# Optimization experiments

Hardware: AMD Instinct MI355X
Metric: run time of the kernel (lower is better)

The kernel has to match this reference:

```python
import jax, jax.numpy as jnp
import numpy as np

SPIN_LEN = 365
TRAIN_LEN = 200000
ML = 2.9086  # mean of second forcing (hard-coded in the torch module)
SL = 1.898   # std of second forcing (hard-coded in the torch module)


def setup_inputs() -> dict:
    key = jax.random.key(0)
    kx, ky, kp = jax.random.split(key, 3)
    B, S = 262144, 1
    x = jax.random.uniform(kx, (B, S, 2), dtype=jnp.float32)
    y_obs = jax.random.uniform(ky, (B, 1), dtype=jnp.float32)
    ks = jax.random.split(kp, 6)
    return {
        "x": x,
        "y_obs": y_obs,
        "epoch": 1,
        "time_lag": 0,
        "weight_r_yom": jax.random.uniform(ks[0], (1, 1), dtype=jnp.float32),
        "weight_r_yom_gw": jax.random.uniform(ks[1], (1, 1), dtype=jnp.float32),
        "weight_r_ylm": jax.random.uniform(ks[2], (1, 1), dtype=jnp.float32),
        "weight_r_yfm": jax.random.uniform(ks[3], (1, 1), dtype=jnp.float32),
        "bias_b0_ylm": jax.random.uniform(ks[4], (1,), dtype=jnp.float32),
        "weight_b2_ylm": jax.random.uniform(ks[5], (1, 1), dtype=jnp.float32),
    }


def reference(x, y_obs, epoch, time_lag, weight_r_yom, weight_r_yom_gw,
              weight_r_ylm, weight_r_yfm, bias_b0_ylm, weight_b2_ylm):
    # x: [B, S, 2] (batch_first). The torch code transposes to [S, B, 2] and
    # runs b-outer / t-inner loops with state threaded across BOTH loops, so
    # the scan order over flattened steps is b-major, t-minor.
    B, S, _ = x.shape
    dt = x.dtype

    # softmax-like mass-balance gate normalization over the 4 scalar weights
    e_om = jnp.exp(weight_r_yom[0, 0])
    e_gw = jnp.exp(weight_r_yom_gw[0, 0])
    e_lm = jnp.exp(weight_r_ylm[0, 0])
    e_fm = jnp.exp(weight_r_yfm[0, 0])
    denom = e_om + e_gw + e_lm + e_fm
    oo = e_om / denom      # constant output gate
    oogw = e_gw / denom    # constant groundwater gate
    ol1 = e_lm / denom     # loss-gate scale
    b0 = bias_b0_ylm[0]
    wb2 = weight_b2_ylm[0, 0]

    # unbiased std, matching torch.std default
    obsstd = jnp.std(y_obs[SPIN_LEN:TRAIN_LEN], ddof=1)

    xv = x[time_lag:]                       # [B', S, 2] (time_lag is static)
    Bp = B - time_lag
    u1 = xv[..., 0].reshape(-1)             # [B'*S] inflow
    u2 = xv[..., 1].reshape(-1)             # [B'*S] loss forcing

    def step(c, u):
        u1_t, u2_t = u
        ol = ol1 * jax.nn.sigmoid(b0 + (u2_t - ML) / SL * wb2)
        f = 1.0 - oo - ol - oogw
        c_new = f * c + u1_t                # ib = 0 -> full inflow enters
        return c_new, (c, ol, f)

    _, (c_prev, ol_s, f_s) = jax.lax.scan(step, jnp.zeros((), dt), (u1, u2))

    # torch stores outputs every t but overwrites; only last t per b survives,
    # using c_0 (state BEFORE that step) and that step's ol/f.
    c0 = c_prev.reshape(Bp, S)[:, -1]
    olL = ol_s.reshape(Bp, S)[:, -1]
    fL = f_s.reshape(Bp, S)[:, -1]

    def pad(v):  # rows b < time_lag stay zero, shape [B, 1]
        return jnp.pad(v, (time_lag, 0))[:, None]

    h_n = pad(oo * c0)          # bp = 0 so h_n == q_n
    c_n = pad(c0)
    l_n = pad(olL * c0)
    gw_n = pad(oogw * c0)
    bp_n = jnp.zeros((B, 1), dt)
    gate_ib = jnp.zeros((B, 1), dt)
    valid = pad(jnp.ones((Bp,), dt))
    gate_oo = oo * valid
    gate_oogw = oogw * valid
    gate_ol = pad(olL)
    gate_f = pad(fL)
    obs_std = obsstd * valid
    h_nout = jnp.concatenate([h_n, obs_std], axis=1)
    return (h_n, c_n, l_n, gw_n, bp_n, gate_ib, gate_oo, gate_oogw,
            gate_ol, gate_f, h_nout, obs_std)
```

## Files before the change

kernel.cpp:

```cpp
#include <hip/hip_runtime.h>
#include <math.h>

#define SPIN 365
#define TRAINL 200000
#define ML 2.9086f
#define SLINV (1.0f / 1.898f)

#define THREADS 512
#define ITEMS 2
#define CHUNK (THREADS * ITEMS)
#define NW (THREADS / 64)

struct Sc { float oo, oogw, ol1, b0, k; };

__device__ __forceinline__ Sc get_sc(const float* w0, const float* w1,
                                     const float* w2, const float* w3,
                                     const float* b0p, const float* wb2p) {
  float e_om = __expf(w0[0]);
  float e_gw = __expf(w1[0]);
  float e_lm = __expf(w2[0]);
  float e_fm = __expf(w3[0]);
  float denom = e_om + e_gw + e_lm + e_fm;
  Sc s;
  s.oo   = e_om / denom;
  s.oogw = e_gw / denom;
  s.ol1  = e_lm / denom;
  s.b0   = b0p[0];
  s.k    = wb2p[0] * SLINV;
  return s;
}

__device__ __forceinline__ float sigm_fast(float z) {
  return __fdividef(1.0f, 1.0f + __expf(-z));
}


extern "C" __global__ __launch_bounds__(THREADS) void k1(
    const float* __restrict__ x, const float* __restrict__ y,
    const int* __restrict__ tlp,
    const float* __restrict__ w0, const float* __restrict__ w1,
    const float* __restrict__ w2, const float* __restrict__ w3,
    const float* __restrict__ b0p, const float* __restrict__ wb2p,
    float* __restrict__ out, float* __restrict__ ws, int B, int G)
{
  const int g = blockIdx.x, tid = threadIdx.x;
  const int lane = tid & 63, wid = tid >> 6;
  const int tl = tlp[0];
  const Sc sc = get_sc(w0, w1, w2, w3, b0p, wb2p);
  const int base = g * CHUNK + tid * ITEMS;
  const bool full = (base + ITEMS) <= B;

  float u1v[ITEMS], u2v[ITEMS];
  if (full) {
    float4 a = *(const float4*)(x + 2 * (size_t)base);
    u1v[0] = a.x; u2v[0] = a.y; u1v[1] = a.z; u2v[1] = a.w;
  } else {
    for (int j = 0; j < ITEMS; j++) {
      int p = base + j;
      u1v[j] = (p < B) ? x[2*(size_t)p]     : 0.f;
      u2v[j] = (p < B) ? x[2*(size_t)p + 1] : 0.f;
    }
  }

  float P = 1.f, Q = 0.f;
  float olv[ITEMS], fv[ITEMS];
  for (int j = 0; j < ITEMS; j++) {
    int p = base + j;
    float ol = sc.ol1 * sigm_fast(sc.b0 + (u2v[j] - ML) * sc.k);
    float f  = 1.0f - sc.oo - ol - sc.oogw;
    olv[j] = ol; fv[j] = f;
    bool act = (p >= tl) && (p < B);
    if (act) { Q = f * Q + u1v[j]; P *= f; }
  }

  if (full) {
    bool a0 = (base >= tl), a1 = (base + 1 >= tl);
    *(float2*)(out + 4*(size_t)B + base) = make_float2(0.f, 0.f);
    *(float2*)(out + 5*(size_t)B + base) = make_float2(0.f, 0.f);
    *(float2*)(out + 6*(size_t)B + base) = make_float2(a0?sc.oo:0.f,  a1?sc.oo:0.f);
    *(float2*)(out + 7*(size_t)B + base) = make_float2(a0?sc.oogw:0.f,a1?sc.oogw:0.f);
    *(float2*)(out + 8*(size_t)B + base) = make_float2(a0?olv[0]:0.f, a1?olv[1]:0.f);
    *(float2*)(out + 9*(size_t)B + base) = make_float2(a0?fv[0]:0.f,  a1?fv[1]:0.f);
  } else {
    for (int j = 0; j < ITEMS; j++) {
      int p = base + j;
      if (p < B) {
        bool act = (p >= tl);
        out[4*(size_t)B+p] = 0.f;                  out[5*(size_t)B+p] = 0.f;
        out[6*(size_t)B+p] = act ? sc.oo   : 0.f;  out[7*(size_t)B+p] = act ? sc.oogw : 0.f;
        out[8*(size_t)B+p] = act ? olv[j]  : 0.f;  out[9*(size_t)B+p] = act ? fv[j]   : 0.f;
      }
    }
  }

  #pragma unroll
  for (int off = 1; off < 64; off <<= 1) {
    float pL = __shfl_down(P, off);
    float qL = __shfl_down(Q, off);
    Q = pL * Q + qL;
    P = pL * P;
  }

  float s = 0.f, ss = 0.f;
  if (full && base < TRAINL) {
    float2 yv = *(const float2*)(y + base);
    float vv[2] = { yv.x, yv.y };
    for (int j = 0; j < ITEMS; j++) {
      int p = base + j;
      if (p >= SPIN && p < TRAINL) { s += vv[j]; ss += vv[j]*vv[j]; }
    }
  } else {
    for (int j = 0; j < ITEMS; j++) {
      int p = base + j;
      if (p >= SPIN && p < TRAINL && p < B) { float v = y[p]; s += v; ss += v*v; }
    }
  }
  #pragma unroll
  for (int off = 1; off < 64; off <<= 1) {
    s  += __shfl_xor(s,  off);
    ss += __shfl_xor(ss, off);
  }

  __shared__ float wA[NW], wB[NW], rS[NW], rSS[NW];
  if (lane == 0) { wA[wid] = P; wB[wid] = Q; rS[wid] = s; rSS[wid] = ss; }
  __syncthreads();
  if (tid == 0) {
    float A = 1.f, Bq = 0.f, S = 0.f, SS = 0.f;
    #pragma unroll
    for (int w = 0; w < NW; w++) {
      Bq = wA[w] * Bq + wB[w];
      A  = wA[w] * A;
      S += rS[w]; SS += rSS[w];
    }
    ws[g] = A; ws[G + g] = Bq; ws[2*G + g] = S; ws[3*G + g] = SS;
  }
}

extern "C" __global__ __launch_bounds__(THREADS) void k2(
    const float* __restrict__ x, const int* __restrict__ tlp,
    const float* __restrict__ w0, const float* __restrict__ w1,
    const float* __restrict__ w2, const float* __restrict__ w3,
    const float* __restrict__ b0p, const float* __restrict__ wb2p,
    float* __restrict__ out, const float* __restrict__ ws, int B, int G)
{
  const int g = blockIdx.x, tid = threadIdx.x;
  const int lane = tid & 63, wid = tid >> 6;
  const int tl = tlp[0];
  const Sc sc = get_sc(w0, w1, w2, w3, b0p, wb2p);
  const int base = g * CHUNK + tid * ITEMS;
  const bool full = (base + ITEMS) <= B;

  float u1v[ITEMS], u2v[ITEMS];
  if (full) {
    float4 a = *(const float4*)(x + 2 * (size_t)base);
    u1v[0] = a.x; u2v[0] = a.y; u1v[1] = a.z; u2v[1] = a.w;
  } else {
    for (int j = 0; j < ITEMS; j++) {
      int p = base + j;
      u1v[j] = (p < B) ? x[2*(size_t)p]     : 0.f;
      u2v[j] = (p < B) ? x[2*(size_t)p + 1] : 0.f;
    }
  }
  float P = 1.f, Q = 0.f;
  float olv[ITEMS], fv[ITEMS];
  for (int j = 0; j < ITEMS; j++) {
    int p = base + j;
    float ol = sc.ol1 * sigm_fast(sc.b0 + (u2v[j] - ML) * sc.k);
    float f  = 1.0f - sc.oo - ol - sc.oogw;
    olv[j] = ol; fv[j] = f;
    bool act = (p >= tl) && (p < B);
    if (act) { Q = f * Q + u1v[j]; P *= f; }
  }

  float iP = P, iQ = Q;
  #pragma unroll
  for (int off = 1; off < 64; off <<= 1) {
    float pa = __shfl_up(iP, off);
    float pb = __shfl_up(iQ, off);
    if (lane >= off) { iQ = iP * pb + iQ; iP = iP * pa; }
  }

  float aP  = (tid < G) ? ws[tid]       : 1.f;
  float aQ  = (tid < G) ? ws[G + tid]   : 0.f;
  float ys  = (tid < G) ? ws[2*G + tid] : 0.f;
  float yss = (tid < G) ? ws[3*G + tid] : 0.f;

  float jP = aP, jQ = aQ;
  #pragma unroll
  for (int off = 1; off < 64; off <<= 1) {
    float pa = __shfl_up(jP, off);
    float pb = __shfl_up(jQ, off);
    if (lane >= off) { jQ = jP * pb + jQ; jP = jP * pa; }
  }

  #pragma unroll
  for (int off = 1; off < 64; off <<= 1) {
    ys  += __shfl_xor(ys,  off);
    yss += __shfl_xor(yss, off);
  }

  __shared__ float wOA[NW], wOB[NW];
  __shared__ float wAA[NW], wAB[NW];
  __shared__ float rS[NW], rSS[NW];
  __shared__ float sQ[THREADS];
  if (lane == 63) { wOA[wid] = iP; wOB[wid] = iQ; wAA[wid] = jP; wAB[wid] = jQ; }
  if (lane == 0)  { rS[wid] = ys; rSS[wid] = yss; }
  __syncthreads();

  float OWA = 1.f, OWB = 0.f, AWA = 1.f, AWB = 0.f;
  for (int w = 0; w < wid; w++) {
    OWB = wOA[w] * OWB + wOB[w];  OWA = wOA[w] * OWA;
    AWB = wAA[w] * AWB + wAB[w];  AWA = wAA[w] * AWA;
  }
  sQ[tid] = jP * AWB + jQ;

  float S = 0.f, SS = 0.f;
  #pragma unroll
  for (int w = 0; w < NW; w++) { S += rS[w]; SS += rSS[w]; }
  float n = (float)(TRAINL - SPIN);
  float mean = S / n;
  float var = (SS - n * mean * mean) / (n - 1.0f);
  float ostd = sqrtf(fmaxf(var, 0.f));
  __syncthreads();

  const float Cg = (g == 0) ? 0.f : sQ[g - 1];

  float eP = __shfl_up(iP, 1);
  float eQ = __shfl_up(iQ, 1);
  if (lane == 0) { eP = 1.f; eQ = 0.f; }
  float Ae = eP * OWA;
  float Be = eP * OWB + eQ;

  float c = Ae * Cg + Be;
  float vh[ITEMS], vc[ITEMS], vl[ITEMS], vgw[ITEMS], vos[ITEMS];
  for (int j = 0; j < ITEMS; j++) {
    int p = base + j;
    bool act = (p >= tl) && (p < B);
    float c0 = c;
    vh[j]  = sc.oo * c0;
    vc[j]  = c0;
    vl[j]  = olv[j] * c0;
    vgw[j] = sc.oogw * c0;
    vos[j] = act ? ostd : 0.f;
    if (act) { c = fv[j] * c + u1v[j]; }
  }

  if (full) {
    *(float2*)(out + (size_t)base)        = make_float2(vh[0], vh[1]);
    *(float2*)(out + (size_t)B + base)    = make_float2(vc[0], vc[1]);
    *(float2*)(out + 2*(size_t)B + base)  = make_float2(vl[0], vl[1]);
    *(float2*)(out + 3*(size_t)B + base)  = make_float2(vgw[0], vgw[1]);
    *(float2*)(out + 12*(size_t)B + base) = make_float2(vos[0], vos[1]);
    *(float4*)(out + 10*(size_t)B + 2*(size_t)base) = make_float4(vh[0], vos[0], vh[1], vos[1]);
  } else {
    for (int j = 0; j < ITEMS; j++) {
      int p = base + j;
      if (p < B) {
        out[(size_t)p]            = vh[j];
        out[(size_t)B + p]        = vc[j];
        out[2*(size_t)B + p]      = vl[j];
        out[3*(size_t)B + p]      = vgw[j];
        out[12*(size_t)B + p]     = vos[j];
        out[10*(size_t)B + 2*p]     = vh[j];
        out[10*(size_t)B + 2*p + 1] = vos[j];
      }
    }
  }
}

extern "C" void kernel_launch(void* const* d_in, const int* in_sizes, int n_in,
                              void* d_out, int out_size, void* d_ws, size_t ws_size,
                              hipStream_t stream) {
  const float* x   = (const float*)d_in[0];
  const float* y   = (const float*)d_in[1];
  const int*   tl  = (const int*)d_in[3];
  const float* w0  = (const float*)d_in[4];
  const float* w1  = (const float*)d_in[5];
  const float* w2  = (const float*)d_in[6];
  const float* w3  = (const float*)d_in[7];
  const float* b0  = (const float*)d_in[8];
  const float* wb2 = (const float*)d_in[9];

  float* out = (float*)d_out;
  float* ws  = (float*)d_ws;

  const int B = in_sizes[0] / 2;
  const int G = (B + CHUNK - 1) / CHUNK;

  k1<<<G, THREADS, 0, stream>>>(x, y, tl, w0, w1, w2, w3, b0, wb2, out, ws, B, G);
  k2<<<G, THREADS, 0, stream>>>(x, tl, w0, w1, w2, w3, b0, wb2, out, ws, B, G);
}
```

Before: 80.31 us.

## Halve block size, use nontemporal stores, two block aggregates per thread

```diff
diff --git a/kernel.cpp b/kernel.cpp
--- a/kernel.cpp
+++ b/kernel.cpp
@@ -6,10 +6,13 @@
 #define ML 2.9086f
 #define SLINV (1.0f / 1.898f)
 
-#define THREADS 512
+#define THREADS 256
 #define ITEMS 2
 #define CHUNK (THREADS * ITEMS)
 #define NW (THREADS / 64)
+
+typedef float v2f __attribute__((ext_vector_type(2)));
+typedef float v4f __attribute__((ext_vector_type(4)));
 
 struct Sc { float oo, oogw, ol1, b0, k; };
 
@@ -34,6 +37,15 @@
   return __fdividef(1.0f, 1.0f + __expf(-z));
 }
 
+__device__ __forceinline__ void nts2(float* p, float a, float b) {
+  v2f v = { a, b };
+  __builtin_nontemporal_store(v, (v2f*)p);
+}
+__device__ __forceinline__ void nts4(float* p, float a, float b, float c, float d) {
+  v4f v = { a, b, c, d };
+  __builtin_nontemporal_store(v, (v4f*)p);
+}
+
 
 extern "C" __global__ __launch_bounds__(THREADS) void k1(
     const float* __restrict__ x, const float* __restrict__ y,
@@ -75,12 +87,12 @@
 
   if (full) {
     bool a0 = (base >= tl), a1 = (base + 1 >= tl);
-    *(float2*)(out + 4*(size_t)B + base) = make_float2(0.f, 0.f);
-    *(float2*)(out + 5*(size_t)B + base) = make_float2(0.f, 0.f);
-    *(float2*)(out + 6*(size_t)B + base) = make_float2(a0?sc.oo:0.f,  a1?sc.oo:0.f);
-    *(float2*)(out + 7*(size_t)B + base) = make_float2(a0?sc.oogw:0.f,a1?sc.oogw:0.f);
-    *(float2*)(out + 8*(size_t)B + base) = make_float2(a0?olv[0]:0.f, a1?olv[1]:0.f);
-    *(float2*)(out + 9*(size_t)B + base) = make_float2(a0?fv[0]:0.f,  a1?fv[1]:0.f);
+    nts2(out + 4*(size_t)B + base, 0.f, 0.f);
+    nts2(out + 5*(size_t)B + base, 0.f, 0.f);
+    nts2(out + 6*(size_t)B + base, a0?sc.oo:0.f,   a1?sc.oo:0.f);
+    nts2(out + 7*(size_t)B + base, a0?sc.oogw:0.f, a1?sc.oogw:0.f);
+    nts2(out + 8*(size_t)B + base, a0?olv[0]:0.f,  a1?olv[1]:0.f);
+    nts2(out + 9*(size_t)B + base, a0?fv[0]:0.f,   a1?fv[1]:0.f);
   } else {
     for (int j = 0; j < ITEMS; j++) {
       int p = base + j;
@@ -146,9 +158,19 @@
   const int g = blockIdx.x, tid = threadIdx.x;
   const int lane = tid & 63, wid = tid >> 6;
   const int tl = tlp[0];
+  const int YB = min(G, (TRAINL + CHUNK - 1) / CHUNK);
   const Sc sc = get_sc(w0, w1, w2, w3, b0p, wb2p);
   const int base = g * CHUNK + tid * ITEMS;
   const bool full = (base + ITEMS) <= B;
+
+  const int i0 = 2 * tid, i1 = 2 * tid + 1;
+  float aP0 = (i0 < G) ? ws[i0]     : 1.f;
+  float aQ0 = (i0 < G) ? ws[G + i0] : 0.f;
+  float aP1 = (i1 < G) ? ws[i1]     : 1.f;
+  float aQ1 = (i1 < G) ? ws[G + i1] : 0.f;
+  float yS  = ((tid)       < YB) ? ws[2*G + tid]       : 0.f;
+  float ySS = ((tid)       < YB) ? ws[3*G + tid]       : 0.f;
+  if (tid + THREADS < YB) { yS += ws[2*G + THREADS + tid]; ySS += ws[3*G + THREADS + tid]; }
 
   float u1v[ITEMS], u2v[ITEMS];
   if (full) {
@@ -180,12 +202,9 @@
     if (lane >= off) { iQ = iP * pb + iQ; iP = iP * pa; }
   }
 
-  float aP  = (tid < G) ? ws[tid]       : 1.f;
-  float aQ  = (tid < G) ? ws[G + tid]   : 0.f;
-  float ys  = (tid < G) ? ws[2*G + tid] : 0.f;
-  float yss = (tid < G) ? ws[3*G + tid] : 0.f;
-
-  float jP = aP, jQ = aQ;
+  float cP = aP1 * aP0;
+  float cQ = aP1 * aQ0 + aQ1;
+  float jP = cP, jQ = cQ;
   #pragma unroll
   for (int off = 1; off < 64; off <<= 1) {
     float pa = __shfl_up(jP, off);
@@ -195,31 +214,39 @@
 
   #pragma unroll
   for (int off = 1; off < 64; off <<= 1) {
-    ys  += __shfl_xor(ys,  off);
-    yss += __shfl_xor(yss, off);
+    yS  += __shfl_xor(yS,  off);
+    ySS += __shfl_xor(ySS, off);
   }
 
   __shared__ float wOA[NW], wOB[NW];
   __shared__ float wAA[NW], wAB[NW];
   __shared__ float rS[NW], rSS[NW];
-  __shared__ float sQ[THREADS];
+  __shared__ float sQ[2 * THREADS];
   if (lane == 63) { wOA[wid] = iP; wOB[wid] = iQ; wAA[wid] = jP; wAB[wid] = jQ; }
-  if (lane == 0)  { rS[wid] = ys; rSS[wid] = yss; }
+  if (lane == 0)  { rS[wid] = yS; rSS[wid] = ySS; }
   __syncthreads();
 
   float OWA = 1.f, OWB = 0.f, AWA = 1.f, AWB = 0.f;
   for (int w = 0; w < wid; w++) {
-    OWB = wOA[w] * OWB + wOB[w];  OWA = wOA[w] * OWA;
-    AWB = wAA[w] * AWB + wAB[w];  AWA = wAA[w] * AWA;
-  }
-  sQ[tid] = jP * AWB + jQ;
+    OWB = wOA[w] * OWB + wOB[w];  OWA *= wOA[w];
+    AWB = wAA[w] * AWB + wAB[w];  AWA *= wAA[w];
+  }
+
+  float pe = __shfl_up(jP, 1);
+  float qe = __shfl_up(jQ, 1);
+  if (lane == 0) { pe = 1.f; qe = 0.f; }
+  float EQ = pe * AWB + qe;
+  float incQ0 = aP0 * EQ + aQ0;
+  float incQ1 = aP1 * incQ0 + aQ1;
+  sQ[i0] = incQ0;
+  if (i1 < 2 * THREADS) sQ[i1] = incQ1;
 
   float S = 0.f, SS = 0.f;
   #pragma unroll
   for (int w = 0; w < NW; w++) { S += rS[w]; SS += rSS[w]; }
-  float n = (float)(TRAINL - SPIN);
-  float mean = S / n;
-  float var = (SS - n * mean * mean) / (n - 1.0f);
+  float nY = (float)(TRAINL - SPIN);
+  float mean = S / nY;
+  float var = (SS - nY * mean * mean) / (nY - 1.0f);
   float ostd = sqrtf(fmaxf(var, 0.f));
   __syncthreads();
 
@@ -228,8 +255,8 @@
   float eP = __shfl_up(iP, 1);
   float eQ = __shfl_up(iQ, 1);
   if (lane == 0) { eP = 1.f; eQ = 0.f; }
-  float Ae = eP * OWA;
-  float Be = eP * OWB + eQ;
+  const float Ae = eP * OWA;
+  const float Be = eP * OWB + eQ;
 
   float c = Ae * Cg + Be;
   float vh[ITEMS], vc[ITEMS], vl[ITEMS], vgw[ITEMS], vos[ITEMS];
@@ -246,12 +273,12 @@
   }
 
   if (full) {
-    *(float2*)(out + (size_t)base)        = make_float2(vh[0], vh[1]);
-    *(float2*)(out + (size_t)B + base)    = make_float2(vc[0], vc[1]);
-    *(float2*)(out + 2*(size_t)B + base)  = make_float2(vl[0], vl[1]);
-    *(float2*)(out + 3*(size_t)B + base)  = make_float2(vgw[0], vgw[1]);
-    *(float2*)(out + 12*(size_t)B + base) = make_float2(vos[0], vos[1]);
-    *(float4*)(out + 10*(size_t)B + 2*(size_t)base) = make_float4(vh[0], vos[0], vh[1], vos[1]);
+    nts2(out + (size_t)base,        vh[0],  vh[1]);
+    nts2(out + (size_t)B + base,    vc[0],  vc[1]);
+    nts2(out + 2*(size_t)B + base,  vl[0],  vl[1]);
+    nts2(out + 3*(size_t)B + base,  vgw[0], vgw[1]);
+    nts2(out + 12*(size_t)B + base, vos[0], vos[1]);
+    nts4(out + 10*(size_t)B + 2*(size_t)base, vh[0], vos[0], vh[1], vos[1]);
   } else {
     for (int j = 0; j < ITEMS; j++) {
       int p = base + j;
```

Result: no change. 81.68 us (+1.7%).
